# Kernel tuning notes

Measured on AMD Instinct MI355X. Metric: run time of the kernel, lower is better.

## Reference

```python
import jax, jax.numpy as jnp
import numpy as np

NU, EU = 40000, 640000          # user-graph nodes / edges
B, T, NW, ET = 64, 16, 30, 60    # users, tweets/user, words/tweet, edges/tweet
NT = B * T * NW                  # 30720 tweet word-nodes
NTE = B * T * ET                 # 61440 tweet edges
NSEG_T = B * T                   # 1024 tweet segments


def gcn_conv(x, src, dst, W, b, N):
    """PyG GCNConv: x@W, add self loops, sym deg-normalize, scatter-add, +b."""
    x = x @ W
    loop = jnp.arange(N)
    s = jnp.concatenate([src, loop])
    d = jnp.concatenate([dst, loop])
    deg = jax.ops.segment_sum(jnp.ones_like(d, dtype=x.dtype), d, num_segments=N)
    dinv = jnp.where(deg > 0, jax.lax.rsqrt(deg), 0.0)
    norm = dinv[s] * dinv[d]                     # [E+N]
    out = jax.ops.segment_sum(x[s] * norm[:, None], d, num_segments=N)
    return out + b


def att_pool(x, seg, nseg, W1, b1, W2, b2):
    """AttentionalAggregation: gate_nn = Linear->Linear, segment softmax, weighted sum."""
    gate = (x @ W1 + b1) @ W2 + b2               # [N, C]
    m = jax.ops.segment_max(gate, seg, num_segments=nseg)
    e = jnp.exp(gate - m[seg])
    s = jax.ops.segment_sum(e, seg, num_segments=nseg)
    a = e / (s[seg] + 1e-16)
    return jax.ops.segment_sum(a * x, seg, num_segments=nseg)  # [nseg, C]


def gru_last(x_seq, W_ih, W_hh, b_ih, b_hh):
    """torch.nn.GRU, 1 layer; x_seq [B,T,C] -> final hidden [B,C]."""
    C = W_hh.shape[1]
    h0 = jnp.zeros((x_seq.shape[0], C), x_seq.dtype)
    def step(h, x):
        gi = x @ W_ih.T + b_ih
        gh = h @ W_hh.T + b_hh
        ir, iz, inn = jnp.split(gi, 3, axis=-1)
        hr, hz, hn = jnp.split(gh, 3, axis=-1)
        r = jax.nn.sigmoid(ir + hr)
        z = jax.nn.sigmoid(iz + hz)
        n = jnp.tanh(inn + r * hn)
        return (1.0 - z) * n + z * h, None
    hT, _ = jax.lax.scan(step, h0, jnp.swapaxes(x_seq, 0, 1))
    return hT


def setup_inputs():
    ks = jax.random.split(jax.random.key(0), 24)
    def rn(i, shape, s=1.0):
        return jax.random.normal(ks[i], shape, dtype=jnp.float32) * s
    z = lambda n_: jnp.zeros((n_,), jnp.float32)
    inp = {}
    inp["user_x"] = rn(0, (NU, 128))
    inp["user_feats"] = rn(1, (B, 32))
    inp["tweet_x"] = rn(2, (NT, 768))
    inp["Wu0"] = rn(3, (128, 128), 0.1); inp["bu0"] = z(128)
    inp["Wu1"] = rn(4, (128, 128), 0.1); inp["bu1"] = z(128)
    inp["Wgu1"] = rn(5, (128, 128), 0.1); inp["bgu1"] = z(128)
    inp["Wgu2"] = rn(6, (128, 128), 0.1); inp["bgu2"] = z(128)
    inp["Wt0"] = rn(7, (768, 256), 0.05); inp["bt0"] = z(256)
    inp["Wt1"] = rn(8, (256, 128), 0.1); inp["bt1"] = z(128)
    inp["Wgt1"] = rn(9, (128, 128), 0.1); inp["bgt1"] = z(128)
    inp["Wgt2"] = rn(10, (128, 128), 0.1); inp["bgt2"] = z(128)
    inp["W_ih"] = rn(11, (384, 128), 0.1); inp["b_ih"] = z(384)
    inp["W_hh"] = rn(12, (384, 128), 0.1); inp["b_hh"] = z(384)
    inp["Wd0"] = rn(13, (288, 256), 0.1); inp["bd0"] = z(256)
    inp["Wd1"] = rn(14, (256, 64), 0.1); inp["bd1"] = z(64)
    inp["Wp"] = rn(15, (64, 1), 0.1); inp["bp"] = z(1)
    inp["user_edge_index"] = jax.random.randint(ks[16], (2, EU), 0, NU)
    local = jax.random.randint(ks[17], (2, NTE), 0, NW)
    offs = jnp.repeat(jnp.arange(NSEG_T) * NW, ET)   # edges stay inside each tweet
    inp["tweet_edge_index"] = local + offs[None, :]
    inp["user_batch"] = jnp.arange(NU) // (NU // B)  # contiguous per-user segments (ptr)
    inp["tweet_batch"] = jnp.arange(NT) // NW        # contiguous per-tweet segments (ptr)
    return inp


def reference(user_x, user_feats, tweet_x,
              Wu0, bu0, Wu1, bu1, Wgu1, bgu1, Wgu2, bgu2,
              Wt0, bt0, Wt1, bt1, Wgt1, bgt1, Wgt2, bgt2,
              W_ih, b_ih, W_hh, b_hh,
              Wd0, bd0, Wd1, bd1, Wp, bp,
              user_edge_index, tweet_edge_index, user_batch, tweet_batch):
    h = jax.nn.relu(gcn_conv(user_x, user_edge_index[0], user_edge_index[1], Wu0, bu0, NU))
    h = jax.nn.relu(gcn_conv(h, user_edge_index[0], user_edge_index[1], Wu1, bu1, NU))
    user_pool = att_pool(h, user_batch, B, Wgu1, bgu1, Wgu2, bgu2)        # [B,128]
    g = jax.nn.relu(gcn_conv(tweet_x, tweet_edge_index[0], tweet_edge_index[1], Wt0, bt0, NT))
    g = jax.nn.relu(gcn_conv(g, tweet_edge_index[0], tweet_edge_index[1], Wt1, bt1, NT))
    tweet_pool = att_pool(g, tweet_batch, NSEG_T, Wgt1, bgt1, Wgt2, bgt2)  # [B*T,128]
    tweet_seq = tweet_pool.reshape(B, T, 128)
    tweet_h = gru_last(tweet_seq, W_ih, W_hh, b_ih, b_hh)                 # [B,128]
    # head
    full = jnp.concatenate([user_feats, user_pool, tweet_h], axis=1)      # [B,288]
    full = jax.nn.relu(full @ Wd0 + bd0)
    full = jax.nn.relu(full @ Wd1 + bd1)
    return jax.nn.sigmoid(full @ Wp + bp)                                 # [B,1]
```

## Files before the change

kernel.cpp:

```cpp
#include <hip/hip_runtime.h>
#include <hip/hip_bf16.h>

#define NU 40000
#define EU 640000
#define BB 64
#define TT 16
#define NW 30
#define NTNODES 30720
#define NTE 61440
#define NSEG_T 1024
#define NCHUNK 16
#define NBU 157
#define NBT 120

typedef __attribute__((ext_vector_type(8))) short bf16x8;
typedef __attribute__((ext_vector_type(4))) float f32x4;

__device__ __forceinline__ unsigned short f2bf(float x) {
    union { float f; unsigned u; } v; v.f = x;
    unsigned r = v.u + 0x7FFFu + ((v.u >> 16) & 1u);
    return (unsigned short)(r >> 16);
}
__device__ __forceinline__ float bf2f(unsigned short u) {
    union { unsigned u; float f; } v; v.u = (unsigned)u << 16; return v.f;
}
__device__ __forceinline__ void gld16(const unsigned short* g, unsigned short* l) {
    __builtin_amdgcn_global_load_lds(
        (const __attribute__((address_space(1))) void*)g,
        (__attribute__((address_space(3))) void*)l, 16, 0, 0);
}

__global__ void k_zeroint(int* __restrict__ p, int n) {
    int i = blockIdx.x * blockDim.x + threadIdx.x;
    if (i < n) p[i] = 0;
}

__global__ void k_hist2(const int* __restrict__ ue_dst, const int* __restrict__ te_dst,
                        int* __restrict__ hist_u, int* __restrict__ hist_t) {
    int i = blockIdx.x * blockDim.x + threadIdx.x;
    if (i < EU) atomicAdd(&hist_u[ue_dst[i]], 1);
    else if (i < EU + NTE) atomicAdd(&hist_t[te_dst[i - EU]], 1);
}

__global__ __launch_bounds__(256) void k_scan_a2(const int* __restrict__ hist_u,
                                                 int* __restrict__ bsum_u,
                                                 int* __restrict__ bsum_t) {
    __shared__ int red[256];
    int b = blockIdx.x, t = threadIdx.x;
    const int* h; int* bs; int n, lb;
    if (b < NBU) { h = hist_u;      bs = bsum_u; n = NU;      lb = b; }
    else         { h = hist_u + NU; bs = bsum_t; n = NTNODES; lb = b - NBU; }
    int i = lb * 256 + t;
    red[t] = (i < n) ? h[i] : 0;
    __syncthreads();
    for (int off = 128; off; off >>= 1) {
        if (t < off) red[t] += red[t + off];
        __syncthreads();
    }
    if (t == 0) bs[lb] = red[0];
}

__global__ __launch_bounds__(256) void k_scan_b2(int* __restrict__ bsum_u,
                                                 int* __restrict__ bsum_t) {
    __shared__ int s[256];
    int t = threadIdx.x;
    int* bs = blockIdx.x ? bsum_t : bsum_u;
    int nb  = blockIdx.x ? NBT : NBU;
    s[t] = (t < nb) ? bs[t] : 0;
    __syncthreads();
    for (int off = 1; off < 256; off <<= 1) {
        int v = (t >= off) ? s[t - off] : 0;
        __syncthreads();
        s[t] += v;
        __syncthreads();
    }
    if (t < nb) bs[t] = (t == 0) ? 0 : s[t - 1];
}

__global__ __launch_bounds__(256) void k_scan_c2(const int* __restrict__ hist_u,
                                                 const int* __restrict__ bsum_u,
                                                 const int* __restrict__ bsum_t,
                                                 int* __restrict__ ptr_u, int* __restrict__ fill_u,
                                                 int* __restrict__ ptr_t, int* __restrict__ fill_t,
                                                 float* __restrict__ dinv_u) {
    __shared__ int s[256];
    int b = blockIdx.x, t = threadIdx.x;
    const int *h, *bs; int *ptr, *fill; int n, lb; float* dv;
    if (b < NBU) { h = hist_u;      bs = bsum_u; ptr = ptr_u; fill = fill_u; n = NU;      lb = b;       dv = dinv_u; }
    else         { h = hist_u + NU; bs = bsum_t; ptr = ptr_t; fill = fill_t; n = NTNODES; lb = b - NBU; dv = dinv_u + NU; }
    int i = lb * 256 + t;
    int hv = (i < n) ? h[i] : 0;
    s[t] = hv;
    __syncthreads();
    for (int off = 1; off < 256; off <<= 1) {
        int v = (t >= off) ? s[t - off] : 0;
        __syncthreads();
        s[t] += v;
        __syncthreads();
    }
    if (i < n) {
        int excl = bs[lb] + s[t] - hv;
        ptr[i] = excl;
        fill[i] = excl;
        dv[i] = rsqrtf((float)hv + 1.0f);
        if (i == n - 1) ptr[n] = excl + hv;
    }
}

__global__ void k_place2(const int* __restrict__ ue_src, const int* __restrict__ ue_dst,
                         const int* __restrict__ te_src, const int* __restrict__ te_dst,
                         int* __restrict__ fill_u, int* __restrict__ esrc_u,
                         int* __restrict__ fill_t, int* __restrict__ esrc_t) {
    int e = blockIdx.x * blockDim.x + threadIdx.x;
    if (e < EU) {
        int pos = atomicAdd(&fill_u[ue_dst[e]], 1);
        esrc_u[pos] = ue_src[e];
    } else if (e < EU + NTE) {
        int e2 = e - EU;
        int pos = atomicAdd(&fill_t[te_dst[e2]], 1);
        esrc_t[pos] = te_src[e2];
    }
}

__device__ __forceinline__ void pack_one(const float* __restrict__ W,
                                         unsigned short* __restrict__ out,
                                         int f, int K, int N, int trans) {
    int j = f & 7;
    int chunk = f >> 3;
    int c = chunk & 511;
    int panel = chunk >> 9;
    int KS = K >> 5;
    int ks = panel % KS;
    int bn = panel / KS;
    int n = bn * 128 + (c & 127);
    int k = ks * 32 + (c >> 7) * 8 + j;
    float v = trans ? W[(size_t)n * K + k] : W[(size_t)k * N + n];
    out[f] = f2bf(v);
}

__global__ void k_packall(const float* __restrict__ Wu0, const float* __restrict__ Wu1,
                          const float* __restrict__ Wgu1, const float* __restrict__ Wgu2,
                          const float* __restrict__ Wt0, const float* __restrict__ Wt1,
                          const float* __restrict__ Wgt1, const float* __restrict__ Wgt2,
                          const float* __restrict__ Wih,
                          const float* __restrict__ Whh, float* __restrict__ whhT,
                          unsigned short* __restrict__ pk) {
    int f = blockIdx.x * blockDim.x + threadIdx.x;
    if (f < 16384)        pack_one(Wu0,  pk + 0,      f,          128, 128, 0);
    else if (f < 32768)   pack_one(Wu1,  pk + 16384,  f - 16384,  128, 128, 0);
    else if (f < 49152)   pack_one(Wgu1, pk + 32768,  f - 32768,  128, 128, 0);
    else if (f < 65536)   pack_one(Wgu2, pk + 49152,  f - 49152,  128, 128, 0);
    else if (f < 262144)  pack_one(Wt0,  pk + 65536,  f - 65536,  768, 256, 0);
    else if (f < 294912)  pack_one(Wt1,  pk + 262144, f - 262144, 256, 128, 0);
    else if (f < 311296)  pack_one(Wgt1, pk + 294912, f - 294912, 128, 128, 0);
    else if (f < 327680)  pack_one(Wgt2, pk + 311296, f - 311296, 128, 128, 0);
    else if (f < 376832)  pack_one(Wih,  pk + 327680, f - 327680, 128, 384, 1);
    else if (f < 425984) {
        int j2 = f - 376832;
        int r = j2 >> 7, k2 = j2 & 127;
        whhT[k2 * 384 + r] = Whh[j2];
    }
}

template<bool AF32>
__global__ __launch_bounds__(256) void k_mgemm(const void* __restrict__ Araw,
                                               const unsigned short* __restrict__ Bpk,
                                               const float* __restrict__ bias,
                                               const float* __restrict__ dscale,
                                               void* __restrict__ Craw,
                                               int M, int K, int N, int flags) {
    constexpr int AST = AF32 ? 260 : 256;
    __shared__ unsigned short Alds[8 * AST];
    __shared__ unsigned short Blds[8192];
    int tid = threadIdx.x, lane = tid & 63, w = tid >> 6;
    int bm = blockIdx.x, bn = blockIdx.y;
    int wr = (w >> 1) * 16, wc = (w & 1) * 64;
    int l15 = lane & 15, lk = lane >> 4;

    f32x4 acc[4];
#pragma unroll
    for (int n = 0; n < 4; ++n) acc[n] = (f32x4){0.f, 0.f, 0.f, 0.f};

    const unsigned short* Bpanel = Bpk + (size_t)bn * (K >> 5) * 4096;
    int KS64 = K >> 6;

    for (int ks = 0; ks < KS64; ++ks) {
        int k0 = ks * 64;
        {
            const unsigned short* bg = Bpanel + (size_t)ks * 8192;
#pragma unroll
            for (int q = 0; q < 4; ++q) {
                int off = (w * 4 + q) * 512;
                gld16(bg + off + lane * 8, &Blds[off]);
            }
        }
        if (AF32) {
            const float* A = (const float*)Araw;
#pragma unroll
            for (int p = 0; p < 2; ++p) {
                int f4 = p * 256 + tid;
                int row = f4 >> 4;
                int kq  = f4 & 15;
                float4 av = *(const float4*)(A + (size_t)(bm * 32 + row) * K + k0 + kq * 4);
                unsigned lo = (unsigned)f2bf(av.x) | ((unsigned)f2bf(av.y) << 16);
                unsigned hi = (unsigned)f2bf(av.z) | ((unsigned)f2bf(av.w) << 16);
                int off = (kq >> 1) * AST + row * 8 + (kq & 1) * 4;
                *(uint2*)&Alds[off] = make_uint2(lo, hi);
            }
        } else {
            const unsigned short* A = (const unsigned short*)Araw;
            int kblk = 2 * w + (lane >> 5);
            int row = lane & 31;
            gld16(A + (size_t)(bm * 32 + row) * K + k0 + kblk * 8,
                  &Alds[w * 512]);
        }
        __syncthreads();
#pragma unroll
        for (int h = 0; h < 2; ++h) {
            int kb = h * 4 + lk;
            bf16x8 a = *(const bf16x8*)&Alds[kb * AST + (wr + l15) * 8];
            bf16x8 b[4];
#pragma unroll
            for (int n = 0; n < 4; ++n)
                b[n] = *(const bf16x8*)&Blds[kb * 1024 + (wc + n * 16 + l15) * 8];
#pragma unroll
            for (int n = 0; n < 4; ++n)
                acc[n] = __builtin_amdgcn_mfma_f32_16x16x32_bf16(a, b[n], acc[n], 0, 0, 0);
        }
        __syncthreads();
    }

    int grow0 = bm * 32 + wr + lk * 4;
#pragma unroll
    for (int i = 0; i < 4; ++i) {
        int grow = grow0 + i;
        float ds = dscale ? dscale[grow] : 1.f;
#pragma unroll
        for (int n = 0; n < 4; ++n) {
            int gcol = bn * 128 + wc + n * 16 + l15;
            float v = acc[n][i] * ds;
            if (flags & 1) v += bias[gcol];
            if (flags & 2) v = fmaxf(v, 0.f);
            if (flags & 4) ((float*)Craw)[(size_t)grow * N + gcol] = v;
            else ((unsigned short*)Craw)[(size_t)grow * N + gcol] = f2bf(v);
        }
    }
}

__global__ __launch_bounds__(256) void k_gatepair(const unsigned short* __restrict__ X,
                                                  const unsigned short* __restrict__ W1,
                                                  const float* __restrict__ b1,
                                                  const unsigned short* __restrict__ W2,
                                                  const float* __restrict__ b2,
                                                  unsigned short* __restrict__ outp, int M) {
    __shared__ unsigned short Ax[16 * 512];
    __shared__ unsigned short Wl[8192];
    int tid = threadIdx.x, lane = tid & 63, w = tid >> 6;
    int bm = blockIdx.x;
    int wr = (w >> 1) * 32, wc = (w & 1) * 64;
    int l15 = lane & 15, lk = lane >> 4;

#pragma unroll
    for (int q = 0; q < 4; ++q) {
        int pl = w * 4 + q;
        gld16(X + (size_t)(bm * 64 + lane) * 128 + pl * 8, &Ax[pl * 512]);
    }

    f32x4 acc[2][4];
#pragma unroll
    for (int m = 0; m < 2; ++m)
#pragma unroll
        for (int n = 0; n < 4; ++n) acc[m][n] = (f32x4){0.f, 0.f, 0.f, 0.f};

    for (int ks = 0; ks < 2; ++ks) {
        const unsigned short* wp = W1 + ks * 8192;
#pragma unroll
        for (int q = 0; q < 4; ++q) {
            int off = (w * 4 + q) * 512;
            gld16(wp + off + lane * 8, &Wl[off]);
        }
        __syncthreads();
#pragma unroll
        for (int h = 0; h < 2; ++h) {
            int kb = h * 4 + lk;
            bf16x8 a[2], b[4];
#pragma unroll
            for (int m = 0; m < 2; ++m)
                a[m] = *(const bf16x8*)&Ax[(ks * 8 + kb) * 512 + (wr + m * 16 + l15) * 8];
#pragma unroll
            for (int n = 0; n < 4; ++n)
                b[n] = *(const bf16x8*)&Wl[kb * 1024 + (wc + n * 16 + l15) * 8];
#pragma unroll
            for (int m = 0; m < 2; ++m)
#pragma unroll
                for (int n = 0; n < 4; ++n)
                    acc[m][n] = __builtin_amdgcn_mfma_f32_16x16x32_bf16(a[m], b[n], acc[m][n], 0, 0, 0);
        }
        __syncthreads();
    }

#pragma unroll
    for (int m = 0; m < 2; ++m)
#pragma unroll
        for (int n = 0; n < 4; ++n) {
            int col = wc + n * 16 + l15;
            float bv = b1[col];
#pragma unroll
            for (int i = 0; i < 4; ++i) {
                int row = wr + m * 16 + lk * 4 + i;
                float v = acc[m][n][i] + bv;
                Ax[(col >> 3) * 512 + row * 8 + (col & 7)] = f2bf(v);
            }
        }
    __syncthreads();

#pragma unroll
    for (int m = 0; m < 2; ++m)
#pragma unroll
        for (int n = 0; n < 4; ++n) acc[m][n] = (f32x4){0.f, 0.f, 0.f, 0.f};
    for (int ks = 0; ks < 2; ++ks) {
        const unsigned short* wp = W2 + ks * 8192;
#pragma unroll
        for (int q = 0; q < 4; ++q) {
            int off = (w * 4 + q) * 512;
            gld16(wp + off + lane * 8, &Wl[off]);
        }
        __syncthreads();
#pragma unroll
        for (int h = 0; h < 2; ++h) {
            int kb = h * 4 + lk;
            bf16x8 a[2], b[4];
#pragma unroll
            for (int m = 0; m < 2; ++m)
                a[m] = *(const bf16x8*)&Ax[(ks * 8 + kb) * 512 + (wr + m * 16 + l15) * 8];
#pragma unroll
            for (int n = 0; n < 4; ++n)
                b[n] = *(const bf16x8*)&Wl[kb * 1024 + (wc + n * 16 + l15) * 8];
#pragma unroll
            for (int m = 0; m < 2; ++m)
#pragma unroll
                for (int n = 0; n < 4; ++n)
                    acc[m][n] = __builtin_amdgcn_mfma_f32_16x16x32_bf16(a[m], b[n], acc[m][n], 0, 0, 0);
        }
        __syncthreads();
    }

#pragma unroll
    for (int m = 0; m < 2; ++m)
#pragma unroll
        for (int n = 0; n < 4; ++n) {
            int col = wc + n * 16 + l15;
            float bv = b2[col];
#pragma unroll
            for (int i = 0; i < 4; ++i) {
                int row = bm * 64 + wr + m * 16 + lk * 4 + i;
                float v = acc[m][n][i] + bv;
                outp[(size_t)row * 128 + col] = f2bf(v);
            }
        }
}

__global__ __launch_bounds__(256) void k_gagg(const unsigned short* __restrict__ y,
                                              const int* __restrict__ ptr,
                                              const int* __restrict__ esrc,
                                              const float* __restrict__ dinv,
                                              const float* __restrict__ bias,
                                              unsigned short* __restrict__ ob, int N, int nch) {
    int idx = blockIdx.x * 4 + (threadIdx.x >> 6);
    if (idx >= N * nch) return;
    int v = idx / nch, ch = idx - v * nch;
    int C = nch << 7;
    int lane = threadIdx.x & 63;
    int c0 = (ch << 7) + lane * 2;
    unsigned yv = *(const unsigned*)(y + (size_t)v * C + c0);
    float a0 = bf2f((unsigned short)yv);
    float a1 = bf2f((unsigned short)(yv >> 16));
    int e = ptr[v], e1 = ptr[v + 1];
    for (; e + 3 < e1; e += 4) {
        int s0 = esrc[e], s1 = esrc[e + 1], s2 = esrc[e + 2], s3 = esrc[e + 3];
        unsigned w0 = *(const unsigned*)(y + (size_t)s0 * C + c0);
        unsigned w1 = *(const unsigned*)(y + (size_t)s1 * C + c0);
        unsigned w2 = *(const unsigned*)(y + (size_t)s2 * C + c0);
        unsigned w3 = *(const unsigned*)(y + (size_t)s3 * C + c0);
        a0 += bf2f((unsigned short)w0) + bf2f((unsigned short)w1)
            + bf2f((unsigned short)w2) + bf2f((unsigned short)w3);
        a1 += bf2f((unsigned short)(w0 >> 16)) + bf2f((unsigned short)(w1 >> 16))
            + bf2f((unsigned short)(w2 >> 16)) + bf2f((unsigned short)(w3 >> 16));
    }
    for (; e < e1; ++e) {
        int s0 = esrc[e];
        unsigned w0 = *(const unsigned*)(y + (size_t)s0 * C + c0);
        a0 += bf2f((unsigned short)w0);
        a1 += bf2f((unsigned short)(w0 >> 16));
    }
    float dv = dinv[v];
    a0 = fmaxf(dv * a0 + bias[c0], 0.f);
    a1 = fmaxf(dv * a1 + bias[c0 + 1], 0.f);
    *(unsigned*)(ob + (size_t)v * C + c0) = (unsigned)f2bf(a0) | ((unsigned)f2bf(a1) << 16);
}

__global__ __launch_bounds__(128) void k_attpool(const unsigned short* __restrict__ x,
                                                 const unsigned short* __restrict__ gate,
                                                 unsigned short* __restrict__ outb, int S) {
    int seg = blockIdx.x;
    int c = threadIdx.x;
    size_t base = (size_t)seg * S * 128 + c;
    float m = -1e30f;
    for (int n = 0; n < S; ++n) m = fmaxf(m, bf2f(gate[base + (size_t)n * 128]));
    float se = 0.f, acc = 0.f;
    for (int n = 0; n < S; ++n) {
        float g = bf2f(gate[base + (size_t)n * 128]);
        float e = expf(g - m);
        se += e;
        acc += e * bf2f(x[base + (size_t)n * 128]);
    }
    outb[(size_t)seg * 128 + c] = f2bf(acc / (se + 1e-16f));
}

__global__ __launch_bounds__(256) void k_pool_pmax(const unsigned short* __restrict__ gate,
                                                   float* __restrict__ pmax, int S) {
    int seg = blockIdx.x, ch = blockIdx.y;
    int c = threadIdx.x & 127, j = threadIdx.x >> 7;
    int csz = (S + NCHUNK - 1) / NCHUNK;
    int n0 = ch * csz, n1 = min(S, n0 + csz);
    size_t base = (size_t)seg * S * 128 + c;
    float m = -1e30f;
    for (int n = n0 + j; n < n1; n += 2)
        m = fmaxf(m, bf2f(gate[base + (size_t)n * 128]));
    __shared__ float red[2][128];
    red[j][c] = m;
    __syncthreads();
    if (j == 0)
        pmax[((size_t)seg * NCHUNK + ch) * 128 + c] = fmaxf(red[0][c], red[1][c]);
}

__global__ __launch_bounds__(256) void k_pool_psum(const unsigned short* __restrict__ x,
                                                   const unsigned short* __restrict__ gate,
                                                   const float* __restrict__ pmax,
                                                   float* __restrict__ pse,
                                                   float* __restrict__ pacc, int S) {
    int seg = blockIdx.x, ch = blockIdx.y;
    int c = threadIdx.x & 127, j = threadIdx.x >> 7;
    int csz = (S + NCHUNK - 1) / NCHUNK;
    int n0 = ch * csz, n1 = min(S, n0 + csz);
    size_t base = (size_t)seg * S * 128 + c;
    float m = -1e30f;
#pragma unroll
    for (int ch2 = 0; ch2 < NCHUNK; ++ch2)
        m = fmaxf(m, pmax[((size_t)seg * NCHUNK + ch2) * 128 + c]);
    float se = 0.f, acc = 0.f;
    for (int n = n0 + j; n < n1; n += 2) {
        float g = bf2f(gate[base + (size_t)n * 128]);
        float e = expf(g - m);
        se += e;
        acc += e * bf2f(x[base + (size_t)n * 128]);
    }
    __shared__ float rs[2][128], ra[2][128];
    rs[j][c] = se; ra[j][c] = acc;
    __syncthreads();
    if (j == 0) {
        size_t o = ((size_t)seg * NCHUNK + ch) * 128 + c;
        pse[o]  = rs[0][c] + rs[1][c];
        pacc[o] = ra[0][c] + ra[1][c];
    }
}

__global__ __launch_bounds__(128) void k_pool_final(const float* __restrict__ pse,
                                                    const float* __restrict__ pacc,
                                                    float* __restrict__ out) {
    int seg = blockIdx.x, c = threadIdx.x;
    float se = 0.f, acc = 0.f;
    for (int ch = 0; ch < NCHUNK; ++ch) {
        size_t o = ((size_t)seg * NCHUNK + ch) * 128 + c;
        se += pse[o];
        acc += pacc[o];
    }
    out[(size_t)seg * 128 + c] = acc / (se + 1e-16f);
}

__global__ __launch_bounds__(768) void k_gru_rec(const float* __restrict__ gi,
                                                 const float* __restrict__ whhT,
                                                 const float* __restrict__ bhh,
                                                 float* __restrict__ hT) {
    __shared__ float hs[128];
    __shared__ float ph[768];
    int b = blockIdx.x, t = threadIdx.x;
    int half = (t >= 384) ? 1 : 0;
    int j = t - half * 384;
    float w[64];
#pragma unroll
    for (int i = 0; i < 64; ++i)
        w[i] = whhT[(half * 64 + i) * 384 + j];
    float chr = 0.f, chz = 0.f, chn = 0.f;
    if (t < 128) {
        hs[t] = 0.f;
        chr = bhh[t]; chz = bhh[128 + t]; chn = bhh[256 + t];
    }
    __syncthreads();
    for (int step = 0; step < TT; ++step) {
        float a0 = 0.f, a1 = 0.f, a2 = 0.f, a3 = 0.f;
        const float* hbase = hs + half * 64;
#pragma unroll
        for (int i = 0; i < 64; i += 4) {
            float4 hv = *(const float4*)(hbase + i);
            a0 += hv.x * w[i + 0];
            a1 += hv.y * w[i + 1];
            a2 += hv.z * w[i + 2];
            a3 += hv.w * w[i + 3];
        }
        ph[t] = (a0 + a1) + (a2 + a3);
        __syncthreads();
        float hnew = 0.f;
        if (t < 128) {
            const float* girow = gi + ((size_t)b * TT + step) * 384;
            float hr = ph[t] + ph[t + 384] + chr;
            float hz = ph[128 + t] + ph[512 + t] + chz;
            float hn = ph[256 + t] + ph[640 + t] + chn;
            float ir = girow[t], iz = girow[128 + t], in = girow[256 + t];
            float r = 1.f / (1.f + expf(-(ir + hr)));
            float z = 1.f / (1.f + expf(-(iz + hz)));
            float n = tanhf(in + r * hn);
            hnew = (1.f - z) * n + z * hs[t];
        }
        __syncthreads();
        if (t < 128) hs[t] = hnew;
        __syncthreads();
    }
    if (t < 128) hT[(size_t)b * 128 + t] = hs[t];
}

__global__ __launch_bounds__(256) void k_head(const float* __restrict__ uf,
                                              const float* __restrict__ up,
                                              const float* __restrict__ th,
                                              const float* __restrict__ Wd0, const float* __restrict__ bd0,
                                              const float* __restrict__ Wd1, const float* __restrict__ bd1,
                                              const float* __restrict__ Wp, const float* __restrict__ bp,
                                              float* __restrict__ out) {
    __shared__ float in0[288], l1[256], l2[64];
    int b = blockIdx.x, t = threadIdx.x;
    if (t < 32) in0[t] = uf[b * 32 + t];
    else if (t < 160) in0[t] = up[b * 128 + (t - 32)];
    if (t < 128) in0[160 + t] = th[b * 128 + t];
    __syncthreads();
    float acc = bd0[t];
    for (int k = 0; k < 288; ++k) acc += in0[k] * Wd0[k * 256 + t];
    l1[t] = fmaxf(acc, 0.f);
    __syncthreads();
    if (t < 64) {
        float a2 = bd1[t];
        for (int k = 0; k < 256; ++k) a2 += l1[k] * Wd1[k * 64 + t];
        l2[t] = fmaxf(a2, 0.f);
    }
    __syncthreads();
    if (t < 64) {
        float p = l2[t] * Wp[t];
        for (int off = 32; off; off >>= 1) p += __shfl_down(p, off, 64);
        if (t == 0) out[b] = 1.f / (1.f + expf(-(p + bp[0])));
    }
}

extern "C" void kernel_launch(void* const* d_in, const int* in_sizes, int n_in,
                              void* d_out, int out_size, void* d_ws, size_t ws_size,
                              hipStream_t stream) {
    const float* user_x     = (const float*)d_in[0];
    const float* user_feats = (const float*)d_in[1];
    const float* tweet_x    = (const float*)d_in[2];
    const float* Wu0 = (const float*)d_in[3];  const float* bu0 = (const float*)d_in[4];
    const float* Wu1 = (const float*)d_in[5];  const float* bu1 = (const float*)d_in[6];
    const float* Wgu1 = (const float*)d_in[7]; const float* bgu1 = (const float*)d_in[8];
    const float* Wgu2 = (const float*)d_in[9]; const float* bgu2 = (const float*)d_in[10];
    const float* Wt0 = (const float*)d_in[11]; const float* bt0 = (const float*)d_in[12];
    const float* Wt1 = (const float*)d_in[13]; const float* bt1 = (const float*)d_in[14];
    const float* Wgt1 = (const float*)d_in[15]; const float* bgt1 = (const float*)d_in[16];
    const float* Wgt2 = (const float*)d_in[17]; const float* bgt2 = (const float*)d_in[18];
    const float* W_ih = (const float*)d_in[19]; const float* b_ih = (const float*)d_in[20];
    const float* W_hh = (const float*)d_in[21]; const float* b_hh = (const float*)d_in[22];
    const float* Wd0 = (const float*)d_in[23]; const float* bd0 = (const float*)d_in[24];
    const float* Wd1 = (const float*)d_in[25]; const float* bd1 = (const float*)d_in[26];
    const float* Wp  = (const float*)d_in[27]; const float* bp  = (const float*)d_in[28];
    const int* ue = (const int*)d_in[29];
    const int* te = (const int*)d_in[30];
    const int* ue_src = ue, *ue_dst = ue + EU;
    const int* te_src = te, *te_dst = te + NTE;

    float* ws = (float*)d_ws;
    size_t o = 0;
    float* dinv_u = ws + o;     o += NU;
    float* dinv_t = ws + o;     o += NTNODES;
    float* user_pool = ws + o;  o += (size_t)BB * 128;
    float* tweet_h = ws + o;    o += (size_t)BB * 128;
    float* whhT = ws + o;       o += 128 * 384;
    float* gi = ws + o;         o += (size_t)NSEG_T * 384;
    float* pmax = ws + o;       o += 131072;
    float* pse = ws + o;        o += 131072;
    float* pacc = ws + o;       o += 131072;
    int* iw = (int*)(ws + o);
    int* hist_u = iw;
    int* hist_t = iw + NU;
    int* ptr_u  = iw + NU + NTNODES;
    int* fill_u = ptr_u + NU + 1;
    int* esrc_u = fill_u + NU;
    int* ptr_t  = esrc_u + EU;
    int* fill_t = ptr_t + NTNODES + 1;
    int* esrc_t = fill_t + NTNODES;
    int* bsum_u = esrc_t + NTE;
    int* bsum_t = bsum_u + 256;
    unsigned short* pk = (unsigned short*)(((uintptr_t)(bsum_t + 256) + 15) & ~(uintptr_t)15);
    unsigned short* pWu0  = pk;
    unsigned short* pWu1  = pWu0  + 16384;
    unsigned short* pWgu1 = pWu1  + 16384;
    unsigned short* pWgu2 = pWgu1 + 16384;
    unsigned short* pWt0  = pWgu2 + 16384;
    unsigned short* pWt1  = pWt0  + 196608;
    unsigned short* pWgt1 = pWt1  + 32768;
    unsigned short* pWgt2 = pWgt1 + 16384;
    unsigned short* pWih  = pWgt2 + 16384;
    unsigned short* arena = (unsigned short*)(((uintptr_t)(pWih + 49152) + 15) & ~(uintptr_t)15);
    const size_t SLOT = (size_t)NTNODES * 256;
    unsigned short* P0 = arena;
    unsigned short* P1 = P0 + SLOT;
    unsigned short* P2 = P1 + SLOT;
    unsigned short* P3 = P2 + SLOT;
    unsigned short* tpool_bf = P3 + SLOT;
    float* out = (float*)d_out;

    dim3 b256(256);
    const int GMU = NU / 32;
    const int GMT = NTNODES / 32;
    const float* NB = nullptr;
    const float* ND = nullptr;

    hipLaunchKernelGGL(k_packall, dim3((425984 + 255) / 256), b256, 0, stream,
                       Wu0, Wu1, Wgu1, Wgu2, Wt0, Wt1, Wgt1, Wgt2, W_ih, W_hh, whhT, pk);

    hipLaunchKernelGGL(k_zeroint, dim3((NU + NTNODES + 255) / 256), b256, 0, stream,
                       hist_u, NU + NTNODES);
    hipLaunchKernelGGL(k_hist2, dim3((EU + NTE + 255) / 256), b256, 0, stream,
                       ue_dst, te_dst, hist_u, hist_t);
    hipLaunchKernelGGL(k_scan_a2, dim3(NBU + NBT), b256, 0, stream, hist_u, bsum_u, bsum_t);
    hipLaunchKernelGGL(k_scan_b2, dim3(2), b256, 0, stream, bsum_u, bsum_t);
    hipLaunchKernelGGL(k_scan_c2, dim3(NBU + NBT), b256, 0, stream,
                       hist_u, bsum_u, bsum_t, ptr_u, fill_u, ptr_t, fill_t, dinv_u);
    hipLaunchKernelGGL(k_place2, dim3((EU + NTE + 255) / 256), b256, 0, stream,
                       ue_src, ue_dst, te_src, te_dst, fill_u, esrc_u, fill_t, esrc_t);

    hipLaunchKernelGGL(HIP_KERNEL_NAME(k_mgemm<true>), dim3(GMT, 2), b256, 0, stream,
                       (const void*)tweet_x, pWt0, NB, dinv_t, (void*)P0, NTNODES, 768, 256, 0);
    hipLaunchKernelGGL(k_gagg, dim3((NTNODES * 2 + 3) / 4), b256, 0, stream,
                       P0, ptr_t, esrc_t, dinv_t, bt0, P1, NTNODES, 2);

    hipLaunchKernelGGL(HIP_KERNEL_NAME(k_mgemm<true>), dim3(GMU, 1), b256, 0, stream,
                       (const void*)user_x, pWu0, NB, dinv_u, (void*)P3, NU, 128, 128, 0);
    hipLaunchKernelGGL(k_gagg, dim3((NU + 3) / 4), b256, 0, stream,
                       P3, ptr_u, esrc_u, dinv_u, bu0, P0, NU, 1);
    hipLaunchKernelGGL(HIP_KERNEL_NAME(k_mgemm<false>), dim3(GMU, 1), b256, 0, stream,
                       (const void*)P0, pWu1, NB, dinv_u, (void*)P2, NU, 128, 128, 0);
    hipLaunchKernelGGL(k_gagg, dim3((NU + 3) / 4), b256, 0, stream,
                       P2, ptr_u, esrc_u, dinv_u, bu1, P3, NU, 1);
    hipLaunchKernelGGL(k_gatepair, dim3(NU / 64), b256, 0, stream,
                       P3, pWgu1, bgu1, pWgu2, bgu2, P0, NU);
    hipLaunchKernelGGL(k_pool_pmax, dim3(BB, NCHUNK), b256, 0, stream, P0, pmax, NU / BB);
    hipLaunchKernelGGL(k_pool_psum, dim3(BB, NCHUNK), b256, 0, stream,
                       P3, P0, pmax, pse, pacc, NU / BB);
    hipLaunchKernelGGL(k_pool_final, dim3(BB), dim3(128), 0, stream, pse, pacc, user_pool);

    hipLaunchKernelGGL(HIP_KERNEL_NAME(k_mgemm<false>), dim3(GMT, 1), b256, 0, stream,
                       (const void*)P1, pWt1, NB, dinv_t, (void*)P2, NTNODES, 256, 128, 0);
    hipLaunchKernelGGL(k_gagg, dim3((NTNODES + 3) / 4), b256, 0, stream,
                       P2, ptr_t, esrc_t, dinv_t, bt1, P3, NTNODES, 1);
    hipLaunchKernelGGL(k_gatepair, dim3(NTNODES / 64), b256, 0, stream,
                       P3, pWgt1, bgt1, pWgt2, bgt2, P1, NTNODES);
    hipLaunchKernelGGL(k_attpool, dim3(NSEG_T), dim3(128), 0, stream,
                       P3, P1, tpool_bf, NW);

    hipLaunchKernelGGL(HIP_KERNEL_NAME(k_mgemm<false>), dim3(NSEG_T / 32, 3), b256, 0, stream,
                       (const void*)tpool_bf, pWih, b_ih, ND, (void*)gi, NSEG_T, 128, 384, 5);
    hipLaunchKernelGGL(k_gru_rec, dim3(BB), dim3(768), 0, stream,
                       gi, whhT, b_hh, tweet_h);

    hipLaunchKernelGGL(k_head, dim3(BB), b256, 0, stream,
                       user_feats, user_pool, tweet_h,
                       Wd0, bd0, Wd1, bd1, Wp, bp, out);
}
```

Before: 347.5 us.

## Merge user and tweet GCN branches into shared dual-problem kernel launches

Replaces the separate per-branch GEMM, aggregation and gate-pair launches with combined kernels that split the grid between the tweet and user problems, so both branches run concurrently in one launch per stage. The point is to cut launch count and fill the GPU better where one branch alone underutilizes it. Buffer assignments are reshuffled so the two branches can share scratch slots. The cost is idle blocks in the shorter half of the grid and extra branching per block.

```diff
diff --git a/kernel.cpp b/kernel.cpp
--- a/kernel.cpp
+++ b/kernel.cpp
@@ -163,17 +163,16 @@
 }
 
 template<bool AF32>
-__global__ __launch_bounds__(256) void k_mgemm(const void* __restrict__ Araw,
-                                               const unsigned short* __restrict__ Bpk,
-                                               const float* __restrict__ bias,
-                                               const float* __restrict__ dscale,
-                                               void* __restrict__ Craw,
-                                               int M, int K, int N, int flags) {
+__device__ __forceinline__ void mgemm_body(const void* __restrict__ Araw,
+                                           const unsigned short* __restrict__ Bpk,
+                                           const float* __restrict__ bias,
+                                           const float* __restrict__ dscale,
+                                           void* __restrict__ Craw,
+                                           int M, int K, int N, int flags,
+                                           int bm, int bn,
+                                           unsigned short* Alds, unsigned short* Blds) {
     constexpr int AST = AF32 ? 260 : 256;
-    __shared__ unsigned short Alds[8 * AST];
-    __shared__ unsigned short Blds[8192];
     int tid = threadIdx.x, lane = tid & 63, w = tid >> 6;
-    int bm = blockIdx.x, bn = blockIdx.y;
     int wr = (w >> 1) * 16, wc = (w & 1) * 64;
     int l15 = lane & 15, lk = lane >> 4;
 
@@ -247,16 +246,52 @@
     }
 }
 
-__global__ __launch_bounds__(256) void k_gatepair(const unsigned short* __restrict__ X,
-                                                  const unsigned short* __restrict__ W1,
-                                                  const float* __restrict__ b1,
-                                                  const unsigned short* __restrict__ W2,
-                                                  const float* __restrict__ b2,
-                                                  unsigned short* __restrict__ outp, int M) {
-    __shared__ unsigned short Ax[16 * 512];
-    __shared__ unsigned short Wl[8192];
+template<bool AF32>
+__global__ __launch_bounds__(256) void k_mgemm(const void* __restrict__ Araw,
+                                               const unsigned short* __restrict__ Bpk,
+                                               const float* __restrict__ bias,
+                                               const float* __restrict__ dscale,
+                                               void* __restrict__ Craw,
+                                               int M, int K, int N, int flags) {
+    constexpr int AST = AF32 ? 260 : 256;
+    __shared__ unsigned short Alds[8 * AST];
+    __shared__ unsigned short Blds[8192];
+    if (blockIdx.x * 32 >= M) return;
+    mgemm_body<AF32>(Araw, Bpk, bias, dscale, Craw, M, K, N, flags,
+                     blockIdx.x, blockIdx.y, Alds, Blds);
+}
+
+template<bool AF32>
+__global__ __launch_bounds__(256) void k_mgemm_dual(
+        const void* __restrict__ A0, const unsigned short* __restrict__ B0,
+        const float* __restrict__ ds0, void* __restrict__ C0, int M0, int K0, int N0,
+        const void* __restrict__ A1, const unsigned short* __restrict__ B1,
+        const float* __restrict__ ds1, void* __restrict__ C1, int M1, int K1, int N1,
+        int bnSplit) {
+    constexpr int AST = AF32 ? 260 : 256;
+    __shared__ unsigned short Alds[8 * AST];
+    __shared__ unsigned short Blds[8192];
+    int bn = blockIdx.y, bm = blockIdx.x;
+    if (bn < bnSplit) {
+        if (bm * 32 >= M0) return;
+        mgemm_body<AF32>(A0, B0, (const float*)nullptr, ds0, C0, M0, K0, N0, 0,
+                         bm, bn, Alds, Blds);
+    } else {
+        if (bm * 32 >= M1) return;
+        mgemm_body<AF32>(A1, B1, (const float*)nullptr, ds1, C1, M1, K1, N1, 0,
+                         bm, bn - bnSplit, Alds, Blds);
+    }
+}
+
+__device__ __forceinline__ void gatepair_body(const unsigned short* __restrict__ X,
+                                              const unsigned short* __restrict__ W1,
+                                              const float* __restrict__ b1,
+                                              const unsigned short* __restrict__ W2,
+                                              const float* __restrict__ b2,
+                                              unsigned short* __restrict__ outp,
+                                              int bm,
+                                              unsigned short* Ax, unsigned short* Wl) {
     int tid = threadIdx.x, lane = tid & 63, w = tid >> 6;
-    int bm = blockIdx.x;
     int wr = (w >> 1) * 32, wc = (w & 1) * 64;
     int l15 = lane & 15, lk = lane >> 4;
 
@@ -360,17 +395,29 @@
         }
 }
 
-__global__ __launch_bounds__(256) void k_gagg(const unsigned short* __restrict__ y,
-                                              const int* __restrict__ ptr,
-                                              const int* __restrict__ esrc,
-                                              const float* __restrict__ dinv,
-                                              const float* __restrict__ bias,
-                                              unsigned short* __restrict__ ob, int N, int nch) {
-    int idx = blockIdx.x * 4 + (threadIdx.x >> 6);
-    if (idx >= N * nch) return;
+__global__ __launch_bounds__(256) void k_gatepair2(
+        const unsigned short* __restrict__ X0, const unsigned short* __restrict__ W10,
+        const float* __restrict__ b10, const unsigned short* __restrict__ W20,
+        const float* __restrict__ b20, unsigned short* __restrict__ O0, int nb0,
+        const unsigned short* __restrict__ X1, const unsigned short* __restrict__ W11,
+        const float* __restrict__ b11, const unsigned short* __restrict__ W21,
+        const float* __restrict__ b21, unsigned short* __restrict__ O1) {
+    __shared__ unsigned short Ax[16 * 512];
+    __shared__ unsigned short Wl[8192];
+    int b = blockIdx.x;
+    if (b < nb0) gatepair_body(X0, W10, b10, W20, b20, O0, b, Ax, Wl);
+    else         gatepair_body(X1, W11, b11, W21, b21, O1, b - nb0, Ax, Wl);
+}
+
+__device__ __forceinline__ void gagg_body(const unsigned short* __restrict__ y,
+                                          const int* __restrict__ ptr,
+                                          const int* __restrict__ esrc,
+                                          const float* __restrict__ dinv,
+                                          const float* __restrict__ bias,
+                                          unsigned short* __restrict__ ob,
+                                          int idx, int nch, int lane) {
     int v = idx / nch, ch = idx - v * nch;
     int C = nch << 7;
-    int lane = threadIdx.x & 63;
     int c0 = (ch << 7) + lane * 2;
     unsigned yv = *(const unsigned*)(y + (size_t)v * C + c0);
     float a0 = bf2f((unsigned short)yv);
@@ -397,6 +444,23 @@
     a0 = fmaxf(dv * a0 + bias[c0], 0.f);
     a1 = fmaxf(dv * a1 + bias[c0 + 1], 0.f);
     *(unsigned*)(ob + (size_t)v * C + c0) = (unsigned)f2bf(a0) | ((unsigned)f2bf(a1) << 16);
+}
+
+__global__ __launch_bounds__(256) void k_gagg2(
+        const unsigned short* __restrict__ y0, const int* __restrict__ ptr0,
+        const int* __restrict__ esrc0, const float* __restrict__ dinv0,
+        const float* __restrict__ bias0, unsigned short* __restrict__ ob0, int N0, int nch0,
+        const unsigned short* __restrict__ y1, const int* __restrict__ ptr1,
+        const int* __restrict__ esrc1, const float* __restrict__ dinv1,
+        const float* __restrict__ bias1, unsigned short* __restrict__ ob1, int N1, int nch1) {
+    int idx = blockIdx.x * 4 + (threadIdx.x >> 6);
+    int lane = threadIdx.x & 63;
+    int T0 = N0 * nch0;
+    if (idx < T0) gagg_body(y0, ptr0, esrc0, dinv0, bias0, ob0, idx, nch0, lane);
+    else {
+        idx -= T0;
+        if (idx < N1 * nch1) gagg_body(y1, ptr1, esrc1, dinv1, bias1, ob1, idx, nch1, lane);
+    }
 }
 
 __global__ __launch_bounds__(128) void k_attpool(const unsigned short* __restrict__ x,
@@ -625,9 +689,6 @@
     float* out = (float*)d_out;
 
     dim3 b256(256);
-    const int GMU = NU / 32;
-    const int GMT = NTNODES / 32;
-    const float* NB = nullptr;
     const float* ND = nullptr;
 
     hipLaunchKernelGGL(k_packall, dim3((425984 + 255) / 256), b256, 0, stream,
@@ -644,34 +705,30 @@
     hipLaunchKernelGGL(k_place2, dim3((EU + NTE + 255) / 256), b256, 0, stream,
                        ue_src, ue_dst, te_src, te_dst, fill_u, esrc_u, fill_t, esrc_t);
 
-    hipLaunchKernelGGL(HIP_KERNEL_NAME(k_mgemm<true>), dim3(GMT, 2), b256, 0, stream,
-                       (const void*)tweet_x, pWt0, NB, dinv_t, (void*)P0, NTNODES, 768, 256, 0);
-    hipLaunchKernelGGL(k_gagg, dim3((NTNODES * 2 + 3) / 4), b256, 0, stream,
-                       P0, ptr_t, esrc_t, dinv_t, bt0, P1, NTNODES, 2);
-
-    hipLaunchKernelGGL(HIP_KERNEL_NAME(k_mgemm<true>), dim3(GMU, 1), b256, 0, stream,
-                       (const void*)user_x, pWu0, NB, dinv_u, (void*)P3, NU, 128, 128, 0);
-    hipLaunchKernelGGL(k_gagg, dim3((NU + 3) / 4), b256, 0, stream,
-                       P3, ptr_u, esrc_u, dinv_u, bu0, P0, NU, 1);
-    hipLaunchKernelGGL(HIP_KERNEL_NAME(k_mgemm<false>), dim3(GMU, 1), b256, 0, stream,
-                       (const void*)P0, pWu1, NB, dinv_u, (void*)P2, NU, 128, 128, 0);
-    hipLaunchKernelGGL(k_gagg, dim3((NU + 3) / 4), b256, 0, stream,
-                       P2, ptr_u, esrc_u, dinv_u, bu1, P3, NU, 1);
-    hipLaunchKernelGGL(k_gatepair, dim3(NU / 64), b256, 0, stream,
-                       P3, pWgu1, bgu1, pWgu2, bgu2, P0, NU);
+    hipLaunchKernelGGL(HIP_KERNEL_NAME(k_mgemm_dual<true>), dim3(NU / 32, 3), b256, 0, stream,
+                       (const void*)tweet_x, pWt0, dinv_t, (void*)P0, NTNODES, 768, 256,
+                       (const void*)user_x,  pWu0, dinv_u, (void*)P2, NU,      128, 128,
+                       2);
+    hipLaunchKernelGGL(k_gagg2, dim3((NTNODES * 2 + NU + 3) / 4), b256, 0, stream,
+                       P0, ptr_t, esrc_t, dinv_t, bt0, P1, NTNODES, 2,
+                       P2, ptr_u, esrc_u, dinv_u, bu0, P3, NU, 1);
+    hipLaunchKernelGGL(HIP_KERNEL_NAME(k_mgemm_dual<false>), dim3(NU / 32, 2), b256, 0, stream,
+                       (const void*)P1, pWt1, dinv_t, (void*)P2, NTNODES, 256, 128,
+                       (const void*)P3, pWu1, dinv_u, (void*)P0, NU,      128, 128,
+                       1);
+    hipLaunchKernelGGL(k_gagg2, dim3((NTNODES + NU + 3) / 4), b256, 0, stream,
+                       P2, ptr_t, esrc_t, dinv_t, bt1, P1, NTNODES, 1,
+                       P0, ptr_u, esrc_u, dinv_u, bu1, P3, NU, 1);
+    hipLaunchKernelGGL(k_gatepair2, dim3(NU / 64 + NTNODES / 64), b256, 0, stream,
+                       P3, pWgu1, bgu1, pWgu2, bgu2, P0, NU / 64,
+                       P1, pWgt1, bgt1, pWgt2, bgt2, P2);
+
     hipLaunchKernelGGL(k_pool_pmax, dim3(BB, NCHUNK), b256, 0, stream, P0, pmax, NU / BB);
     hipLaunchKernelGGL(k_pool_psum, dim3(BB, NCHUNK), b256, 0, stream,
                        P3, P0, pmax, pse, pacc, NU / BB);
     hipLaunchKernelGGL(k_pool_final, dim3(BB), dim3(128), 0, stream, pse, pacc, user_pool);
-
-    hipLaunchKernelGGL(HIP_KERNEL_NAME(k_mgemm<false>), dim3(GMT, 1), b256, 0, stream,
-                       (const void*)P1, pWt1, NB, dinv_t, (void*)P2, NTNODES, 256, 128, 0);
-    hipLaunchKernelGGL(k_gagg, dim3((NTNODES + 3) / 4), b256, 0, stream,
-                       P2, ptr_t, esrc_t, dinv_t, bt1, P3, NTNODES, 1);
-    hipLaunchKernelGGL(k_gatepair, dim3(NTNODES / 64), b256, 0, stream,
-                       P3, pWgt1, bgt1, pWgt2, bgt2, P1, NTNODES);
     hipLaunchKernelGGL(k_attpool, dim3(NSEG_T), dim3(128), 0, stream,
-                       P3, P1, tpool_bf, NW);
+                       P1, P2, tpool_bf, NW);
 
     hipLaunchKernelGGL(HIP_KERNEL_NAME(k_mgemm<false>), dim3(NSEG_T / 32, 3), b256, 0, stream,
                        (const void*)tpool_bf, pWih, b_ih, ND, (void*)gi, NSEG_T, 128, 384, 5);
```

New measurement: 330.6 us, median of 2. 1.05x faster.
